# Kernel optimization log

Hardware: AMD Instinct MI355X
Metric: run time of the kernel (lower is better)

## Reference

```python
import jax, jax.numpy as jnp
import numpy as np

N, E, D, H = 20000, 320000, 64, 8  # nodes, edges, embedding_dim, heads


def setup_inputs() -> dict:
    key = jax.random.key(0)
    ks = jax.random.split(key, 11)
    s = 0.05
    inp = {
        "x": jax.random.normal(ks[0], (N, D), jnp.float32),
        "edge_index": jax.random.randint(ks[1], (2, E), 0, N, jnp.int32),
        # layer 1: GATv2Conv(D, D, heads=H, concat=True)
        "Wl1": jax.random.normal(ks[2], (D, H * D), jnp.float32) * s,
        "Wr1": jax.random.normal(ks[3], (D, H * D), jnp.float32) * s,
        "att1": jax.random.normal(ks[4], (H, D), jnp.float32) * s,
        "b1": jnp.zeros((H * D,), jnp.float32),
        # layer 2: GATv2Conv(H*D, D, heads=H, concat=False)
        "Wl2": jax.random.normal(ks[5], (H * D, H * D), jnp.float32) * s,
        "Wr2": jax.random.normal(ks[6], (H * D, H * D), jnp.float32) * s,
        "att2": jax.random.normal(ks[7], (H, D), jnp.float32) * s,
        "b2": jnp.zeros((D,), jnp.float32),
    }
    return inp


def gatv2_layer(x, Wl, Wr, att, b, src, dst, n, concat):
    """PyG GATv2Conv (eval mode, dropout off). lin_l feeds source msgs, lin_r targets."""
    heads, out_c = att.shape
    xl = (x @ Wl).reshape(n, heads, out_c)   # source-side transform
    xr = (x @ Wr).reshape(n, heads, out_c)   # target-side transform
    e = jax.nn.leaky_relu(xl[src] + xr[dst], negative_slope=0.2)  # [E,H,C]
    logits = jnp.einsum('ehc,hc->eh', e, att)                     # [E,H]
    # numerically-stable segment softmax over incoming edges of each dst node
    m = jax.ops.segment_max(logits, dst, num_segments=n)          # [N,H]
    p = jnp.exp(logits - m[dst])
    denom = jax.ops.segment_sum(p, dst, num_segments=n)           # [N,H]
    alpha = p / denom[dst]                                        # [E,H]
    out = jax.ops.segment_sum(xl[src] * alpha[..., None], dst, num_segments=n)  # [N,H,C]
    out = out.reshape(n, heads * out_c) if concat else out.mean(axis=1)
    return out + b


def reference(x, edge_index, Wl1, Wr1, att1, b1, Wl2, Wr2, att2, b2):
    n = x.shape[0]
    loops = jnp.arange(n, dtype=edge_index.dtype)  # PyG add_self_loops=True
    src = jnp.concatenate([edge_index[0], loops])
    dst = jnp.concatenate([edge_index[1], loops])
    h = gatv2_layer(x, Wl1, Wr1, att1, b1, src, dst, n, concat=True)   # [N, H*D]
    h = jax.nn.elu(h)
    out = gatv2_layer(h, Wl2, Wr2, att2, b2, src, dst, n, concat=False)  # [N, D]
    return out
```

## Files before the change

### kernel.cpp

```cpp
#include <hip/hip_runtime.h>
#include <hip/hip_fp16.h>
#include <math.h>

#define DD 64
#define HH 8
#define HD 512
#define NC 1024

typedef __attribute__((ext_vector_type(8))) short bf16x8;
typedef __attribute__((ext_vector_type(4))) float f32x4;
typedef __attribute__((ext_vector_type(8))) unsigned short ushort8;

__device__ __forceinline__ ushort bf16_rne(float f) {
    uint u = __float_as_uint(f);
    u += 0x7fffu + ((u >> 16) & 1u);
    return (ushort)(u >> 16);
}
__device__ __forceinline__ float bf16_tof(ushort h) {
    return __uint_as_float(((uint)h) << 16);
}
__device__ __forceinline__ float h2f(ushort u) {
    __half h; *reinterpret_cast<ushort*>(&h) = u; return __half2float(h);
}
__device__ __forceinline__ __half2 pk_max(__half2 a, __half2 b) {
    __half2 r;
    asm("v_pk_max_f16 %0, %1, %2" : "=v"(r) : "v"(a), "v"(b));
    return r;
}

__global__ __launch_bounds__(256) void split_mat(const float* __restrict__ in,
                                                 ushort* __restrict__ hi,
                                                 ushort* __restrict__ lo, int total)
{
    const int i = blockIdx.x * 256 + threadIdx.x;
    if (i >= total) return;
    const float f = in[i];
    const ushort h = bf16_rne(f);
    hi[i] = h;
    lo[i] = bf16_rne(f - bf16_tof(h));
}

__global__ __launch_bounds__(256) void split_wT(const float* __restrict__ W0,
                                                const float* __restrict__ W1,
                                                ushort* __restrict__ hi,
                                                ushort* __restrict__ lo, int kshift)
{
    const int K = 1 << kshift;
    const int i = blockIdx.x * 256 + threadIdx.x;
    if (i >= 1024 * K) return;
    const int c = i >> kshift, k = i & (K - 1);
    const float* W = (c < 512) ? W0 : W1;
    const float f = W[(size_t)k * 512 + (c & 511)];
    const ushort h = bf16_rne(f);
    hi[i] = h;
    lo[i] = bf16_rne(f - bf16_tof(h));
}

__global__ __launch_bounds__(256) void gemm_bf16x3(
    const ushort* __restrict__ Ah, const ushort* __restrict__ Al,
    const ushort* __restrict__ Bh, const ushort* __restrict__ Bl,
    __half* __restrict__ C, int M, int K)
{
    __shared__ __align__(16) ushort lAh[128 * 64];
    __shared__ __align__(16) ushort lAl[128 * 64];
    __shared__ __align__(16) ushort lBh[128 * 64];
    __shared__ __align__(16) ushort lBl[128 * 64];

    const int nwg = gridDim.x;
    const int wg  = (blockIdx.x & 7) * (nwg >> 3) + (blockIdx.x >> 3);
    const int ntile = wg & 7, mtile = wg >> 3;
    const int bm = mtile * 128, bn = ntile * 128;

    const int tid  = threadIdx.x;
    const int wid  = tid >> 6;
    const int lane = tid & 63;
    const int wr = wid >> 1, wc = wid & 1;
    const int l15 = lane & 15, g = lane >> 4;

    const int rsub = lane >> 3;
    const int gch  = (lane & 7) ^ rsub;

    f32x4 acc[4][4] = {};

    for (int k0 = 0; k0 < K; k0 += 64) {
        __syncthreads();
        #pragma unroll
        for (int q = 0; q < 4; ++q) {
            const int rowb = wid * 32 + q * 8;
            const int row  = rowb + rsub;
            const size_t ga = (size_t)min(bm + row, M - 1) * K + k0 + gch * 8;
            const size_t gb = (size_t)(bn + row) * K + k0 + gch * 8;
            __builtin_amdgcn_global_load_lds(
                (const __attribute__((address_space(1))) void*)(Ah + ga),
                (__attribute__((address_space(3))) void*)(lAh + rowb * 64), 16, 0, 0);
            __builtin_amdgcn_global_load_lds(
                (const __attribute__((address_space(1))) void*)(Al + ga),
                (__attribute__((address_space(3))) void*)(lAl + rowb * 64), 16, 0, 0);
            __builtin_amdgcn_global_load_lds(
                (const __attribute__((address_space(1))) void*)(Bh + gb),
                (__attribute__((address_space(3))) void*)(lBh + rowb * 64), 16, 0, 0);
            __builtin_amdgcn_global_load_lds(
                (const __attribute__((address_space(1))) void*)(Bl + gb),
                (__attribute__((address_space(3))) void*)(lBl + rowb * 64), 16, 0, 0);
        }
        __syncthreads();

        #pragma unroll
        for (int kk = 0; kk < 2; ++kk) {
            bf16x8 ah[4], al[4], bh[4], bl[4];
            #pragma unroll
            for (int m = 0; m < 4; ++m) {
                const int row = wr * 64 + m * 16 + l15;
                const int sc  = (kk * 4 + g) ^ (row & 7);
                const int idx = row * 64 + (sc << 3);
                ah[m] = *(const bf16x8*)(lAh + idx);
                al[m] = *(const bf16x8*)(lAl + idx);
            }
            #pragma unroll
            for (int n = 0; n < 4; ++n) {
                const int row = wc * 64 + n * 16 + l15;
                const int sc  = (kk * 4 + g) ^ (row & 7);
                const int idx = row * 64 + (sc << 3);
                bh[n] = *(const bf16x8*)(lBh + idx);
                bl[n] = *(const bf16x8*)(lBl + idx);
            }
            #pragma unroll
            for (int m = 0; m < 4; ++m)
                #pragma unroll
                for (int n = 0; n < 4; ++n) {
                    acc[m][n] = __builtin_amdgcn_mfma_f32_16x16x32_bf16(
                                    ah[m], bh[n], acc[m][n], 0, 0, 0);
                    acc[m][n] = __builtin_amdgcn_mfma_f32_16x16x32_bf16(
                                    ah[m], bl[n], acc[m][n], 0, 0, 0);
                    acc[m][n] = __builtin_amdgcn_mfma_f32_16x16x32_bf16(
                                    al[m], bh[n], acc[m][n], 0, 0, 0);
                }
        }
    }

    #pragma unroll
    for (int m = 0; m < 4; ++m) {
        #pragma unroll
        for (int i = 0; i < 4; ++i) {
            const int row = bm + wr * 64 + m * 16 + g * 4 + i;
            if (row >= M) continue;
            __half* cp = C + (size_t)row * NC + bn + wc * 64 + l15;
            #pragma unroll
            for (int n = 0; n < 4; ++n)
                cp[n * 16] = __float2half_rn(acc[m][n][i]);
        }
    }
}

__global__ __launch_bounds__(256) void hist_deg(const int* __restrict__ dsts,
                                                int E, int ET, int* __restrict__ deg)
{
    const int w = blockIdx.x * blockDim.x + threadIdx.x;
    if (w >= ET) return;
    const int d = (w < E) ? dsts[w] : (w - E);
    atomicAdd(&deg[d], 1);
}

__global__ __launch_bounds__(1024) void scan_rowptr(const int* __restrict__ deg,
                                                    int* __restrict__ rowptr,
                                                    int* __restrict__ cursor, int n)
{
    __shared__ int sums[1024];
    const int tid   = threadIdx.x;
    const int chunk = (n + 1023) / 1024;
    const int lo = min(tid * chunk, n), hi = min(lo + chunk, n);

    int s = 0;
    for (int i = lo; i < hi; ++i) s += deg[i];
    sums[tid] = s;
    __syncthreads();

    for (int off = 1; off < 1024; off <<= 1) {
        const int t = (tid >= off) ? sums[tid - off] : 0;
        __syncthreads();
        sums[tid] += t;
        __syncthreads();
    }

    int run = sums[tid] - s;
    for (int i = lo; i < hi; ++i) {
        rowptr[i] = run;
        cursor[i] = run;
        run += deg[i];
    }
    if (tid == 1023) rowptr[n] = run;
}

__global__ __launch_bounds__(256) void scatter_csr(const int* __restrict__ srcs,
                                                   const int* __restrict__ dsts,
                                                   int E, int ET,
                                                   int* __restrict__ cursor,
                                                   int* __restrict__ eidx)
{
    const int w = blockIdx.x * blockDim.x + threadIdx.x;
    if (w >= ET) return;
    int s, d;
    if (w < E) { s = srcs[w]; d = dsts[w]; }
    else       { s = w - E;   d = s; }
    const int pos = atomicAdd(&cursor[d], 1);
    eidx[pos] = s;
}

__device__ __forceinline__ void edge_step_pk(const ushort8 v,
                                             const __half2* __restrict__ ra,
                                             const __half2* __restrict__ at,
                                             const __half2 c02,
                                             float* __restrict__ acc, float& den)
{
    float vf[8];
    __half2 sacc = __floats2half2_rn(0.f, 0.f);
    #pragma unroll
    for (int j = 0; j < 4; ++j) {
        ushort2 u = make_ushort2(v[2 * j], v[2 * j + 1]);
        const __half2 vh = *reinterpret_cast<const __half2*>(&u);
        const float2 vv = __half22float2(vh);
        vf[2 * j] = vv.x; vf[2 * j + 1] = vv.y;
        __half2 t = __hadd2(vh, ra[j]);
        t = pk_max(t, __hmul2(t, c02));
        sacc = __hfma2(t, at[j], sacc);
    }
    float s = __low2float(sacc) + __high2float(sacc);
    s += __shfl_xor(s, 1, 64);
    s += __shfl_xor(s, 2, 64);
    s += __shfl_xor(s, 4, 64);
    const float p = __expf(s);
    den += p;
    #pragma unroll
    for (int j = 0; j < 8; ++j) acc[j] = fmaf(p, vf[j], acc[j]);
}

template<int MODE>
__global__ __launch_bounds__(256) void gat_fused(
    const __half* __restrict__ xlr, const float* __restrict__ att,
    const float* __restrict__ bias, const int* __restrict__ rowptr,
    const int* __restrict__ eidx, int n, float* __restrict__ out,
    ushort* __restrict__ oh, ushort* __restrict__ ol)
{
    const int d    = (blockIdx.x * blockDim.x + threadIdx.x) >> 6;
    const int lane = threadIdx.x & 63;
    if (d >= n) return;

    const int o = lane * 8;
    const __half2 c02 = __floats2half2_rn(0.2f, 0.2f);

    __half2 ra[4], at[4];
    {
        const ushort8 rv = *(const ushort8*)((const ushort*)xlr + (size_t)d * NC + 512 + o);
        #pragma unroll
        for (int j = 0; j < 4; ++j) {
            ushort2 u = make_ushort2(rv[2 * j], rv[2 * j + 1]);
            ra[j] = *reinterpret_cast<const __half2*>(&u);
            at[j] = __floats2half2_rn(att[o + 2 * j], att[o + 2 * j + 1]);
        }
    }

    float acc[8] = {};
    float den = 0.f;

    const int start = rowptr[d];
    const int end   = rowptr[d + 1];
    const int last  = end - 1;
    const ushort* xb = (const ushort*)xlr;

    ushort8 v0 = *(const ushort8*)(xb + ((size_t)eidx[start] << 10) + o);
    ushort8 v1 = *(const ushort8*)(xb + ((size_t)eidx[min(start + 1, last)] << 10) + o);

    int e = start;
    for (; e + 1 < end; e += 2) {
        const int i2 = min(e + 2, last), i3 = min(e + 3, last);
        const ushort8 n0 = *(const ushort8*)(xb + ((size_t)eidx[i2] << 10) + o);
        const ushort8 n1 = *(const ushort8*)(xb + ((size_t)eidx[i3] << 10) + o);
        edge_step_pk(v0, ra, at, c02, acc, den);
        edge_step_pk(v1, ra, at, c02, acc, den);
        v0 = n0; v1 = n1;
    }
    if (e < end) edge_step_pk(v0, ra, at, c02, acc, den);

    const float inv = 1.f / den;

    if (MODE == 0) {
        float bv[8];
        *(float4*)&bv[0] = *(const float4*)(bias + o);
        *(float4*)&bv[4] = *(const float4*)(bias + o + 4);
        ushort8 hx, lx;
        #pragma unroll
        for (int j = 0; j < 8; ++j) {
            const float u = fmaf(acc[j], inv, bv[j]);
            const float w = u > 0.f ? u : expm1f(u);
            const ushort h = bf16_rne(w);
            hx[j] = h;
            lx[j] = bf16_rne(w - bf16_tof(h));
        }
        *(ushort8*)(oh + (size_t)d * HD + o) = hx;
        *(ushort8*)(ol + (size_t)d * HD + o) = lx;
    } else {
        float m[8];
        #pragma unroll
        for (int j = 0; j < 8; ++j) m[j] = acc[j] * inv;
        #pragma unroll
        for (int j = 0; j < 8; ++j) {
            m[j] += __shfl_xor(m[j], 8,  64);
            m[j] += __shfl_xor(m[j], 16, 64);
            m[j] += __shfl_xor(m[j], 32, 64);
        }
        if (lane < 8) {
            const int c = lane * 8;
            float4 r0, r1;
            r0.x = fmaf(m[0], 0.125f, bias[c + 0]);
            r0.y = fmaf(m[1], 0.125f, bias[c + 1]);
            r0.z = fmaf(m[2], 0.125f, bias[c + 2]);
            r0.w = fmaf(m[3], 0.125f, bias[c + 3]);
            r1.x = fmaf(m[4], 0.125f, bias[c + 4]);
            r1.y = fmaf(m[5], 0.125f, bias[c + 5]);
            r1.z = fmaf(m[6], 0.125f, bias[c + 6]);
            r1.w = fmaf(m[7], 0.125f, bias[c + 7]);
            *(float4*)(out + (size_t)d * DD + c)     = r0;
            *(float4*)(out + (size_t)d * DD + c + 4) = r1;
        }
    }
}

extern "C" void kernel_launch(void* const* d_in, const int* in_sizes, int n_in,
                              void* d_out, int out_size, void* d_ws, size_t ws_size,
                              hipStream_t stream)
{
    const float* x    = (const float*)d_in[0];
    const int*   ei   = (const int*)  d_in[1];
    const float* Wl1  = (const float*)d_in[2];
    const float* Wr1  = (const float*)d_in[3];
    const float* att1 = (const float*)d_in[4];
    const float* b1   = (const float*)d_in[5];
    const float* Wl2  = (const float*)d_in[6];
    const float* Wr2  = (const float*)d_in[7];
    const float* att2 = (const float*)d_in[8];
    const float* b2   = (const float*)d_in[9];

    const int N  = in_sizes[0] / DD;
    const int E  = in_sizes[1] / 2;
    const int ET = E + N;

    const int* srcs = ei;
    const int* dsts = ei + E;

    __half* xlr   = (__half*)d_ws;
    ushort* xs_h  = (ushort*)(xlr + (size_t)N * NC);
    ushort* xs_l  = xs_h  + (size_t)N * DD;
    ushort* h1_h  = xs_l  + (size_t)N * DD;
    ushort* h1_l  = h1_h  + (size_t)N * HD;
    ushort* bt1_h = h1_l  + (size_t)N * HD;
    ushort* bt1_l = bt1_h + 1024 * DD;
    ushort* bt2_h = bt1_l + 1024 * DD;
    ushort* bt2_l = bt2_h + 1024 * HD;
    int* rowptr = (int*)(bt2_l + 1024 * HD);
    int* deg    = rowptr + (N + 1);
    int* cursor = deg + N;
    int* eidx   = cursor + N;

    const dim3 gblk(256);
    const int  eblk  = (ET + 255) / 256;
    const int  nblk  = (N + 3) / 4;
    const int  MT    = (N + 127) / 128;
    const int  gemm_grid = 8 * MT;

    hipMemsetAsync(deg, 0, (size_t)N * sizeof(int), stream);
    hist_deg   <<<eblk, gblk, 0, stream>>>(dsts, E, ET, deg);
    scan_rowptr<<<1, 1024, 0, stream>>>(deg, rowptr, cursor, N);
    scatter_csr<<<eblk, gblk, 0, stream>>>(srcs, dsts, E, ET, cursor, eidx);

    split_mat<<<(N * DD + 255) / 256, gblk, 0, stream>>>(x, xs_h, xs_l, N * DD);
    split_wT <<<(1024 * DD + 255) / 256, gblk, 0, stream>>>(Wl1, Wr1, bt1_h, bt1_l, 6);
    split_wT <<<(1024 * HD + 255) / 256, gblk, 0, stream>>>(Wl2, Wr2, bt2_h, bt2_l, 9);

    gemm_bf16x3<<<gemm_grid, gblk, 0, stream>>>(xs_h, xs_l, bt1_h, bt1_l, xlr, N, DD);
    gat_fused<0><<<nblk, gblk, 0, stream>>>(xlr, att1, b1, rowptr, eidx, N,
                                            nullptr, h1_h, h1_l);

    gemm_bf16x3<<<gemm_grid, gblk, 0, stream>>>(h1_h, h1_l, bt2_h, bt2_l, xlr, N, HD);
    gat_fused<1><<<nblk, gblk, 0, stream>>>(xlr, att2, b2, rowptr, eidx, N,
                                            (float*)d_out, nullptr, nullptr);
}
```

Baseline: 279.9 us.

## Merge prep kernels into one launch and deepen edge gather prefetch to four

Folds the x split, both weight transpose-splits and the degree histogram into one multi-role kernel, which removes three launches and lets these independent tasks run concurrently. Separately, the per-node edge loop in the fused GAT kernel now processes four edges per iteration, keeping four row gathers in flight and loading the next indices two stages ahead. The deeper prefetch costs more registers and can lower occupancy. The merged kernel assumes N*D and the weight sizes divide evenly by 256, since it drops the bounds checks.

```diff
diff --git a/kernel.cpp b/kernel.cpp
--- a/kernel.cpp
+++ b/kernel.cpp
@@ -19,41 +19,55 @@
 __device__ __forceinline__ float bf16_tof(ushort h) {
     return __uint_as_float(((uint)h) << 16);
 }
-__device__ __forceinline__ float h2f(ushort u) {
-    __half h; *reinterpret_cast<ushort*>(&h) = u; return __half2float(h);
-}
 __device__ __forceinline__ __half2 pk_max(__half2 a, __half2 b) {
     __half2 r;
     asm("v_pk_max_f16 %0, %1, %2" : "=v"(r) : "v"(a), "v"(b));
     return r;
 }
 
-__global__ __launch_bounds__(256) void split_mat(const float* __restrict__ in,
-                                                 ushort* __restrict__ hi,
-                                                 ushort* __restrict__ lo, int total)
-{
-    const int i = blockIdx.x * 256 + threadIdx.x;
-    if (i >= total) return;
-    const float f = in[i];
-    const ushort h = bf16_rne(f);
-    hi[i] = h;
-    lo[i] = bf16_rne(f - bf16_tof(h));
-}
-
-__global__ __launch_bounds__(256) void split_wT(const float* __restrict__ W0,
-                                                const float* __restrict__ W1,
-                                                ushort* __restrict__ hi,
-                                                ushort* __restrict__ lo, int kshift)
-{
-    const int K = 1 << kshift;
-    const int i = blockIdx.x * 256 + threadIdx.x;
-    if (i >= 1024 * K) return;
-    const int c = i >> kshift, k = i & (K - 1);
-    const float* W = (c < 512) ? W0 : W1;
-    const float f = W[(size_t)k * 512 + (c & 511)];
-    const ushort h = bf16_rne(f);
-    hi[i] = h;
-    lo[i] = bf16_rne(f - bf16_tof(h));
+__global__ __launch_bounds__(256) void prep(
+    const float* __restrict__ x,
+    const float* __restrict__ Wl1, const float* __restrict__ Wr1,
+    const float* __restrict__ Wl2, const float* __restrict__ Wr2,
+    const int* __restrict__ dsts,
+    ushort* __restrict__ xs_h, ushort* __restrict__ xs_l,
+    ushort* __restrict__ bt1_h, ushort* __restrict__ bt1_l,
+    ushort* __restrict__ bt2_h, ushort* __restrict__ bt2_l,
+    int* __restrict__ deg,
+    int N, int E, int ET, int nb_sm, int nb_w1, int nb_w2)
+{
+    const int b   = blockIdx.x;
+    const int tid = threadIdx.x;
+
+    if (b < nb_sm) {
+        const int i = b * 256 + tid;
+        const float f = x[i];
+        const ushort h = bf16_rne(f);
+        xs_h[i] = h;
+        xs_l[i] = bf16_rne(f - bf16_tof(h));
+    } else if (b < nb_sm + nb_w1) {
+        const int i = (b - nb_sm) * 256 + tid;
+        const int c = i >> 6, k = i & 63;
+        const float* W = (c < 512) ? Wl1 : Wr1;
+        const float f = W[(size_t)k * 512 + (c & 511)];
+        const ushort h = bf16_rne(f);
+        bt1_h[i] = h;
+        bt1_l[i] = bf16_rne(f - bf16_tof(h));
+    } else if (b < nb_sm + nb_w1 + nb_w2) {
+        const int i = (b - nb_sm - nb_w1) * 256 + tid;
+        const int c = i >> 9, k = i & 511;
+        const float* W = (c < 512) ? Wl2 : Wr2;
+        const float f = W[(size_t)k * 512 + (c & 511)];
+        const ushort h = bf16_rne(f);
+        bt2_h[i] = h;
+        bt2_l[i] = bf16_rne(f - bf16_tof(h));
+    } else {
+        const int w = (b - nb_sm - nb_w1 - nb_w2) * 256 + tid;
+        if (w < ET) {
+            const int d = (w < E) ? dsts[w] : (w - E);
+            atomicAdd(&deg[d], 1);
+        }
+    }
 }
 
 __global__ __launch_bounds__(256) void gemm_bf16x3(
@@ -152,15 +166,6 @@
     }
 }
 
-__global__ __launch_bounds__(256) void hist_deg(const int* __restrict__ dsts,
-                                                int E, int ET, int* __restrict__ deg)
-{
-    const int w = blockIdx.x * blockDim.x + threadIdx.x;
-    if (w >= ET) return;
-    const int d = (w < E) ? dsts[w] : (w - E);
-    atomicAdd(&deg[d], 1);
-}
-
 __global__ __launch_bounds__(1024) void scan_rowptr(const int* __restrict__ deg,
                                                     int* __restrict__ rowptr,
                                                     int* __restrict__ cursor, int n)
@@ -267,19 +272,45 @@
     const int last  = end - 1;
     const ushort* xb = (const ushort*)xlr;
 
-    ushort8 v0 = *(const ushort8*)(xb + ((size_t)eidx[start] << 10) + o);
-    ushort8 v1 = *(const ushort8*)(xb + ((size_t)eidx[min(start + 1, last)] << 10) + o);
+    ushort8 vA0, vA1, vA2, vA3;
+    int iB0, iB1, iB2, iB3;
+    {
+        const int a0 = eidx[start];
+        const int a1 = eidx[min(start + 1, last)];
+        const int a2 = eidx[min(start + 2, last)];
+        const int a3 = eidx[min(start + 3, last)];
+        vA0 = *(const ushort8*)(xb + ((size_t)a0 << 10) + o);
+        vA1 = *(const ushort8*)(xb + ((size_t)a1 << 10) + o);
+        vA2 = *(const ushort8*)(xb + ((size_t)a2 << 10) + o);
+        vA3 = *(const ushort8*)(xb + ((size_t)a3 << 10) + o);
+        iB0 = eidx[min(start + 4, last)];
+        iB1 = eidx[min(start + 5, last)];
+        iB2 = eidx[min(start + 6, last)];
+        iB3 = eidx[min(start + 7, last)];
+    }
 
     int e = start;
-    for (; e + 1 < end; e += 2) {
-        const int i2 = min(e + 2, last), i3 = min(e + 3, last);
-        const ushort8 n0 = *(const ushort8*)(xb + ((size_t)eidx[i2] << 10) + o);
-        const ushort8 n1 = *(const ushort8*)(xb + ((size_t)eidx[i3] << 10) + o);
-        edge_step_pk(v0, ra, at, c02, acc, den);
-        edge_step_pk(v1, ra, at, c02, acc, den);
-        v0 = n0; v1 = n1;
-    }
-    if (e < end) edge_step_pk(v0, ra, at, c02, acc, den);
+    for (; e + 3 < end; e += 4) {
+        const ushort8 vB0 = *(const ushort8*)(xb + ((size_t)iB0 << 10) + o);
+        const ushort8 vB1 = *(const ushort8*)(xb + ((size_t)iB1 << 10) + o);
+        const ushort8 vB2 = *(const ushort8*)(xb + ((size_t)iB2 << 10) + o);
+        const ushort8 vB3 = *(const ushort8*)(xb + ((size_t)iB3 << 10) + o);
+        const int nB0 = eidx[min(e + 8,  last)];
+        const int nB1 = eidx[min(e + 9,  last)];
+        const int nB2 = eidx[min(e + 10, last)];
+        const int nB3 = eidx[min(e + 11, last)];
+
+        edge_step_pk(vA0, ra, at, c02, acc, den);
+        edge_step_pk(vA1, ra, at, c02, acc, den);
+        edge_step_pk(vA2, ra, at, c02, acc, den);
+        edge_step_pk(vA3, ra, at, c02, acc, den);
+
+        vA0 = vB0; vA1 = vB1; vA2 = vB2; vA3 = vB3;
+        iB0 = nB0; iB1 = nB1; iB2 = nB2; iB3 = nB3;
+    }
+    if (e < end)     edge_step_pk(vA0, ra, at, c02, acc, den);
+    if (e + 1 < end) edge_step_pk(vA1, ra, at, c02, acc, den);
+    if (e + 2 < end) edge_step_pk(vA2, ra, at, c02, acc, den);
 
     const float inv = 1.f / den;
 
@@ -362,19 +393,21 @@
     int* eidx   = cursor + N;
 
     const dim3 gblk(256);
-    const int  eblk  = (ET + 255) / 256;
     const int  nblk  = (N + 3) / 4;
     const int  MT    = (N + 127) / 128;
     const int  gemm_grid = 8 * MT;
 
+    const int nb_sm = (N * DD) / 256;
+    const int nb_w1 = (1024 * DD) / 256;
+    const int nb_w2 = (1024 * HD) / 256;
+    const int nb_h  = (ET + 255) / 256;
+
     hipMemsetAsync(deg, 0, (size_t)N * sizeof(int), stream);
-    hist_deg   <<<eblk, gblk, 0, stream>>>(dsts, E, ET, deg);
+    prep<<<nb_sm + nb_w1 + nb_w2 + nb_h, gblk, 0, stream>>>(
+        x, Wl1, Wr1, Wl2, Wr2, dsts, xs_h, xs_l, bt1_h, bt1_l, bt2_h, bt2_l,
+        deg, N, E, ET, nb_sm, nb_w1, nb_w2);
     scan_rowptr<<<1, 1024, 0, stream>>>(deg, rowptr, cursor, N);
-    scatter_csr<<<eblk, gblk, 0, stream>>>(srcs, dsts, E, ET, cursor, eidx);
-
-    split_mat<<<(N * DD + 255) / 256, gblk, 0, stream>>>(x, xs_h, xs_l, N * DD);
-    split_wT <<<(1024 * DD + 255) / 256, gblk, 0, stream>>>(Wl1, Wr1, bt1_h, bt1_l, 6);
-    split_wT <<<(1024 * HD + 255) / 256, gblk, 0, stream>>>(Wl2, Wr2, bt2_h, bt2_l, 9);
+    scatter_csr<<<nb_h, gblk, 0, stream>>>(srcs, dsts, E, ET, cursor, eidx);
 
     gemm_bf16x3<<<gemm_grid, gblk, 0, stream>>>(xs_h, xs_l, bt1_h, bt1_l, xlr, N, DD);
     gat_fused<0><<<nblk, gblk, 0, stream>>>(xlr, att1, b1, rowptr, eidx, N,
```

After: 280.5 us. No clear change (+0.2%).
